# Performance work log

Measured on AMD Instinct MI355X. Metric: run time of the kernel, lower is better.

Reference implementation:

```python
import jax, jax.numpy as jnp
import numpy as np
from jax import lax

B, T = 8, 256
GRID = (8, 8, 8)
X, Y, Z = GRID
N = X * Y * Z            # 512 nodes
C_IN = C_OUT = 8         # 4096 / 512
R = 8                    # num_rand


def _stencil_mask():
    # 7-point stencil mask at kernel center (1,1,1)
    m = np.zeros((3, 3, 3), dtype=np.float32)
    c = 1
    m[c, c, c] = 1.0
    m[c - 1, c, c] = 1.0
    m[c + 1, c, c] = 1.0
    m[c, c - 1, c] = 1.0
    m[c, c + 1, c] = 1.0
    m[c, c, c - 1] = 1.0
    m[c, c, c + 1] = 1.0
    return jnp.asarray(m)


def setup_inputs() -> dict:
    key = jax.random.key(0)
    k1, k2, k3, k4 = jax.random.split(key, 4)
    x = jax.random.normal(k1, (B, T, C_IN * N), dtype=jnp.float32)
    # MaskedConv3d params (kernel 3x3x3)
    fan = C_IN * 27
    conv_w = jax.random.normal(k2, (C_OUT, C_IN, 3, 3, 3), dtype=jnp.float32) / np.sqrt(fan)
    conv_b = jnp.zeros((C_OUT,), dtype=jnp.float32)
    # RandomGraphMixer3D params (xavier-uniform-like)
    bound = np.sqrt(6.0 / (C_IN * R + C_OUT))
    mix_w = jax.random.uniform(k3, (C_OUT, C_IN, R), jnp.float32, -bound, bound)
    mix_b = jnp.zeros((C_OUT,), dtype=jnp.float32)
    rand_indices = jax.random.randint(k4, (N, R), 0, N, dtype=jnp.int32)
    alpha = jnp.float32(0.5)
    return {"x": x, "conv_w": conv_w, "conv_b": conv_b,
            "mix_w": mix_w, "mix_b": mix_b, "alpha": alpha,
            "rand_indices": rand_indices}


def reference(x, conv_w, conv_b, mix_w, mix_b, alpha, rand_indices):
    Bd, Td, D = x.shape
    xt = x.reshape(Bd * Td, C_IN, X, Y, Z)
    # --- masked 7-point stencil conv3d ---
    w = conv_w * _stencil_mask()  # broadcast over (O, I)
    y_local = lax.conv_general_dilated(
        xt, w, window_strides=(1, 1, 1), padding='SAME',
        dimension_numbers=('NCDHW', 'OIDHW', 'NCDHW'))
    y_local = y_local + conv_b[None, :, None, None, None]
    # --- random graph mixer: gather + contract ---
    x_nodes = xt.reshape(Bd * Td, C_IN, N)
    gathered = x_nodes[:, :, rand_indices]              # [BT, C, N, R]
    y_rand = jnp.einsum('ocr,bcnr->bon', mix_w, gathered) + mix_b[None, :, None]
    y_rand = y_rand.reshape(Bd * Td, C_OUT, X, Y, Z)
    # --- sigmoid blend ---
    a = jax.nn.sigmoid(alpha)
    yt = a * y_local + (1.0 - a) * y_rand
    return yt.reshape(Bd, Td, C_OUT * N)
```

## Files before the change

kernel.cpp:

```cpp
#include <hip/hip_runtime.h>
#include <math.h>

#define NNODES 512
#define CIN 8
#define COUT 8
#define RR 8
#define BTB 2
#define GUARD 64
#define SLOTS (GUARD + NNODES + GUARD)
#define SLAB_HW (SLOTS * 8)
#define LDS_HW (BTB * SLAB_HW)
#define WTAB 1024

typedef __attribute__((ext_vector_type(8))) short short8;
typedef __attribute__((ext_vector_type(4))) float floatx4;

__device__ __forceinline__ unsigned int pack_bf16(float a, float b) {
    unsigned int ua = __float_as_uint(a);
    unsigned int ub = __float_as_uint(b);
    ua = (ua + 0x7fffu + ((ua >> 16) & 1u)) >> 16;
    ub = (ub + 0x7fffu + ((ub >> 16) & 1u)) & 0xffff0000u;
    return ua | ub;
}

__global__ void prep(const float* __restrict__ conv_w,
                     const float* __restrict__ conv_b,
                     const float* __restrict__ mix_w,
                     const float* __restrict__ mix_b,
                     const float* __restrict__ alpha_p,
                     const int*   __restrict__ rand_idx,
                     float* __restrict__ ws) {
    const int t = threadIdx.x;
    const float a = 1.0f / (1.0f + expf(-alpha_p[0]));
    if (t < 960) {
        const int oc = t / 15;
        const int tap = t % 15;
        float v;
        if (tap < 7) {
            const int off[7] = {13, 4, 22, 10, 16, 12, 14};
            v = a * conv_w[oc * 27 + off[tap]];
        } else {
            v = (1.0f - a) * mix_w[oc * RR + (tap - 7)];
        }
        ws[t] = v;
    } else if (t < 968) {
        const int o = t - 960;
        ws[960 + o] = a * conv_b[o] + (1.0f - a) * mix_b[o];
    }

    int4* tab = (int4*)((int*)ws + WTAB);
    for (int e = t; e < 2048; e += 1024) {
        const int tt = e >> 6, lane = e & 63;
        const int q = lane >> 4, r16 = lane & 15;
        const int m = tt * 16 + r16;
        const int h = (m >> 3) & 7, w = m & 7;
        int off[4];
#pragma unroll
        for (int i = 0; i < 4; ++i) {
            const int tap = 4 * i + q;
            int o;
            if (tap == 0)       o = GUARD + m;
            else if (tap == 1)  o = GUARD + m - 64;
            else if (tap == 2)  o = GUARD + m + 64;
            else if (tap == 3)  o = (h > 0) ? (GUARD + m - 8) : 0;
            else if (tap == 4)  o = (h < 7) ? (GUARD + m + 8) : 0;
            else if (tap == 5)  o = (w > 0) ? (GUARD + m - 1) : 0;
            else if (tap == 6)  o = (w < 7) ? (GUARD + m + 1) : 0;
            else if (tap <= 14) o = GUARD + rand_idx[m * RR + (tap - 7)];
            else                o = 0;
            off[i] = o * 16;
        }
        tab[e] = make_int4(off[0], off[1], off[2], off[3]);
    }
}

__global__ __launch_bounds__(256) void hybrid3d_v3(
    const float* __restrict__ x,
    const float* __restrict__ wsb,
    float* __restrict__ out)
{
    __shared__ unsigned short lds16[LDS_HW];
    const int tid  = threadIdx.x;
    const int wave = tid >> 6;
    const int lane = tid & 63;
    const int quad = lane >> 4;
    const int r16  = lane & 15;
    const int btl  = wave >> 1;
    const int half = wave & 1;

    {
        const int b = tid >> 7;
        const int s = tid & 127;
        const int slot = (s < GUARD) ? s : (NNODES + s);
        *(uint4*)&lds16[b * SLAB_HW + slot * 8] = make_uint4(0u, 0u, 0u, 0u);
    }

    short8 bfrag[4];
#pragma unroll
    for (int i = 0; i < 4; ++i) {
        const int tap = 4 * i + quad;
        union { unsigned int u[4]; short8 s; } bf;
#pragma unroll
        for (int jp = 0; jp < 4; ++jp) {
            const int c0 = 2 * jp, c1 = 2 * jp + 1;
            float f0 = (r16 < 8 && tap < 15) ? wsb[(r16 * CIN + c0) * 15 + tap] : 0.0f;
            float f1 = (r16 < 8 && tap < 15) ? wsb[(r16 * CIN + c1) * 15 + tap] : 0.0f;
            bf.u[jp] = pack_bf16(f0, f1);
        }
        bfrag[i] = bf.s;
    }
    const float bias = (r16 < 8) ? wsb[960 + r16] : 0.0f;

    const float* xg = x + ((size_t)blockIdx.x * BTB + btl) * (CIN * NNODES);
    unsigned short* slab = lds16 + btl * SLAB_HW;
#pragma unroll
    for (int j = 0; j < 4; ++j) {
        const int n = half * 256 + j * 64 + lane;
        float v[8];
#pragma unroll
        for (int c = 0; c < 8; ++c) v[c] = xg[c * NNODES + n];
        uint4 pk;
        pk.x = pack_bf16(v[0], v[1]);
        pk.y = pack_bf16(v[2], v[3]);
        pk.z = pack_bf16(v[4], v[5]);
        pk.w = pack_bf16(v[6], v[7]);
        *(uint4*)&slab[(GUARD + n) * 8] = pk;
    }
    __syncthreads();

    const char* slabp = (const char*)slab;
    const int4* tab = (const int4*)((const int*)wsb + WTAB);
    float* outb = out + ((size_t)blockIdx.x * BTB + btl) * (COUT * NNODES);

#pragma unroll 2
    for (int tt = 0; tt < 16; ++tt) {
        const int t = half * 16 + tt;
        const int4 off = tab[t * 64 + lane];
        union { uint4 u; short8 s; } r0, r1, r2, r3;
        r0.u = *(const uint4*)(slabp + off.x);
        r1.u = *(const uint4*)(slabp + off.y);
        r2.u = *(const uint4*)(slabp + off.z);
        r3.u = *(const uint4*)(slabp + off.w);

        floatx4 acc_a = {bias, bias, bias, bias};
        floatx4 acc_b = {0.0f, 0.0f, 0.0f, 0.0f};
        acc_a = __builtin_amdgcn_mfma_f32_16x16x32_bf16(r0.s, bfrag[0], acc_a, 0, 0, 0);
        acc_b = __builtin_amdgcn_mfma_f32_16x16x32_bf16(r2.s, bfrag[2], acc_b, 0, 0, 0);
        acc_a = __builtin_amdgcn_mfma_f32_16x16x32_bf16(r1.s, bfrag[1], acc_a, 0, 0, 0);
        acc_b = __builtin_amdgcn_mfma_f32_16x16x32_bf16(r3.s, bfrag[3], acc_b, 0, 0, 0);

        if (r16 < 8) {
            float4 res;
            res.x = acc_a.x + acc_b.x;
            res.y = acc_a.y + acc_b.y;
            res.z = acc_a.z + acc_b.z;
            res.w = acc_a.w + acc_b.w;
            *(float4*)(outb + r16 * NNODES + t * 16 + quad * 4) = res;
        }
    }
}

extern "C" void kernel_launch(void* const* d_in, const int* in_sizes, int n_in,
                              void* d_out, int out_size, void* d_ws, size_t ws_size,
                              hipStream_t stream) {
    const float* x       = (const float*)d_in[0];
    const float* conv_w  = (const float*)d_in[1];
    const float* conv_b  = (const float*)d_in[2];
    const float* mix_w   = (const float*)d_in[3];
    const float* mix_b   = (const float*)d_in[4];
    const float* alpha_p = (const float*)d_in[5];
    const int*   rand_i  = (const int*)d_in[6];
    float* out = (float*)d_out;
    float* ws  = (float*)d_ws;

    const int BT = in_sizes[0] / (CIN * NNODES);

    prep<<<1, 1024, 0, stream>>>(conv_w, conv_b, mix_w, mix_b, alpha_p, rand_i, ws);
    hybrid3d_v3<<<BT / BTB, 256, 0, stream>>>(x, ws, out);
}
```

Baseline: 105.6 us.

## Fold weight prep and offset table into the main kernel, computing offsets inline

Removes the separate single-block prep kernel. The main kernel now computes the sigmoid-blended bf16 weight fragments and bias directly from the raw parameters, and derives the stencil and random-gather LDS offsets in registers instead of reading a precomputed table. The tap-to-lane mapping is reorganized so each quad handles fixed stencil directions, with the random indices prefetched from rand_idx one iteration ahead. This saves a kernel launch and the serialization between the two kernels, at the cost of redundant weight setup in every block and more integer arithmetic per loop iteration.

```diff
diff --git a/kernel.cpp b/kernel.cpp
--- a/kernel.cpp
+++ b/kernel.cpp
@@ -10,7 +10,6 @@
 #define SLOTS (GUARD + NNODES + GUARD)
 #define SLAB_HW (SLOTS * 8)
 #define LDS_HW (BTB * SLAB_HW)
-#define WTAB 1024
 
 typedef __attribute__((ext_vector_type(8))) short short8;
 typedef __attribute__((ext_vector_type(4))) float floatx4;
@@ -23,60 +22,14 @@
     return ua | ub;
 }
 
-__global__ void prep(const float* __restrict__ conv_w,
-                     const float* __restrict__ conv_b,
-                     const float* __restrict__ mix_w,
-                     const float* __restrict__ mix_b,
-                     const float* __restrict__ alpha_p,
-                     const int*   __restrict__ rand_idx,
-                     float* __restrict__ ws) {
-    const int t = threadIdx.x;
-    const float a = 1.0f / (1.0f + expf(-alpha_p[0]));
-    if (t < 960) {
-        const int oc = t / 15;
-        const int tap = t % 15;
-        float v;
-        if (tap < 7) {
-            const int off[7] = {13, 4, 22, 10, 16, 12, 14};
-            v = a * conv_w[oc * 27 + off[tap]];
-        } else {
-            v = (1.0f - a) * mix_w[oc * RR + (tap - 7)];
-        }
-        ws[t] = v;
-    } else if (t < 968) {
-        const int o = t - 960;
-        ws[960 + o] = a * conv_b[o] + (1.0f - a) * mix_b[o];
-    }
-
-    int4* tab = (int4*)((int*)ws + WTAB);
-    for (int e = t; e < 2048; e += 1024) {
-        const int tt = e >> 6, lane = e & 63;
-        const int q = lane >> 4, r16 = lane & 15;
-        const int m = tt * 16 + r16;
-        const int h = (m >> 3) & 7, w = m & 7;
-        int off[4];
-#pragma unroll
-        for (int i = 0; i < 4; ++i) {
-            const int tap = 4 * i + q;
-            int o;
-            if (tap == 0)       o = GUARD + m;
-            else if (tap == 1)  o = GUARD + m - 64;
-            else if (tap == 2)  o = GUARD + m + 64;
-            else if (tap == 3)  o = (h > 0) ? (GUARD + m - 8) : 0;
-            else if (tap == 4)  o = (h < 7) ? (GUARD + m + 8) : 0;
-            else if (tap == 5)  o = (w > 0) ? (GUARD + m - 1) : 0;
-            else if (tap == 6)  o = (w < 7) ? (GUARD + m + 1) : 0;
-            else if (tap <= 14) o = GUARD + rand_idx[m * RR + (tap - 7)];
-            else                o = 0;
-            off[i] = o * 16;
-        }
-        tab[e] = make_int4(off[0], off[1], off[2], off[3]);
-    }
-}
-
-__global__ __launch_bounds__(256) void hybrid3d_v3(
+__global__ __launch_bounds__(256) void hybrid3d_v4(
     const float* __restrict__ x,
-    const float* __restrict__ wsb,
+    const float* __restrict__ conv_w,
+    const float* __restrict__ conv_b,
+    const float* __restrict__ mix_w,
+    const float* __restrict__ mix_b,
+    const float* __restrict__ alpha_p,
+    const int*   __restrict__ rand_idx,
     float* __restrict__ out)
 {
     __shared__ unsigned short lds16[LDS_HW];
@@ -95,22 +48,6 @@
         *(uint4*)&lds16[b * SLAB_HW + slot * 8] = make_uint4(0u, 0u, 0u, 0u);
     }
 
-    short8 bfrag[4];
-#pragma unroll
-    for (int i = 0; i < 4; ++i) {
-        const int tap = 4 * i + quad;
-        union { unsigned int u[4]; short8 s; } bf;
-#pragma unroll
-        for (int jp = 0; jp < 4; ++jp) {
-            const int c0 = 2 * jp, c1 = 2 * jp + 1;
-            float f0 = (r16 < 8 && tap < 15) ? wsb[(r16 * CIN + c0) * 15 + tap] : 0.0f;
-            float f1 = (r16 < 8 && tap < 15) ? wsb[(r16 * CIN + c1) * 15 + tap] : 0.0f;
-            bf.u[jp] = pack_bf16(f0, f1);
-        }
-        bfrag[i] = bf.s;
-    }
-    const float bias = (r16 < 8) ? wsb[960 + r16] : 0.0f;
-
     const float* xg = x + ((size_t)blockIdx.x * BTB + btl) * (CIN * NNODES);
     unsigned short* slab = lds16 + btl * SLAB_HW;
 #pragma unroll
@@ -126,21 +63,80 @@
         pk.w = pack_bf16(v[6], v[7]);
         *(uint4*)&slab[(GUARD + n) * 8] = pk;
     }
+
+    const float aS = 1.0f / (1.0f + expf(-alpha_p[0]));
+    const float aR = 1.0f - aS;
+    short8 bfrag[4];
+#pragma unroll
+    for (int i = 0; i < 4; ++i) {
+        const int tap = 4 * i + quad;
+        union { unsigned int u[4]; short8 s; } bf;
+#pragma unroll
+        for (int jp = 0; jp < 4; ++jp) {
+            float f0 = 0.0f, f1 = 0.0f;
+            if (r16 < 8) {
+                const int c0 = 2 * jp, c1 = c0 + 1;
+                if (tap < 7) {
+                    const unsigned long long TAB =
+                        13ull | (4ull << 8) | (22ull << 16) | (10ull << 24) |
+                        (16ull << 32) | (12ull << 40) | (14ull << 48);
+                    const int co = (int)((TAB >> (8 * tap)) & 0xffull);
+                    f0 = aS * conv_w[(r16 * CIN + c0) * 27 + co];
+                    f1 = aS * conv_w[(r16 * CIN + c1) * 27 + co];
+                } else if (tap < 15) {
+                    const int r = tap - 7;
+                    f0 = aR * mix_w[(r16 * CIN + c0) * RR + r];
+                    f1 = aR * mix_w[(r16 * CIN + c1) * RR + r];
+                }
+            }
+            bf.u[jp] = pack_bf16(f0, f1);
+        }
+        bfrag[i] = bf.s;
+    }
+    const float bias = (r16 < 8) ? (aS * conv_b[r16] + aR * mix_b[r16]) : 0.0f;
+
     __syncthreads();
 
     const char* slabp = (const char*)slab;
-    const int4* tab = (const int4*)((const int*)wsb + WTAB);
     float* outb = out + ((size_t)blockIdx.x * BTB + btl) * (COUT * NNODES);
+
+    const int  w_  = r16 & 7;
+    const int  hb  = r16 >> 3;
+    const int  j1  = (quad + 1) & 3;
+    const bool q3  = (quad == 3);
+    const int  s0d = (quad == 0) ? 0 : (quad == 1) ? -64 : (quad == 2) ? 64 : -8;
+    const int  s1d = (quad == 0) ? 8 : (quad == 1) ? -1 : 1;
+    const bool c1s = (quad == 1) ? (w_ > 0) : (quad == 2) ? (w_ < 7) : true;
+    const int  base0 = (GUARD + r16 + s0d) * 16;
+    const int  base1 = (GUARD + r16 + s1d) * 16;
+
+    const int* rp = rand_idx + ((half * 16) * 16 + r16) * RR + j1;
+    int nr1 = rp[0], nr2 = rp[4];
 
 #pragma unroll 2
     for (int tt = 0; tt < 16; ++tt) {
         const int t = half * 16 + tt;
-        const int4 off = tab[t * 64 + lane];
+        const int rv1 = nr1, rv2 = nr2;
+        if (tt < 15) { rp += 16 * RR; nr1 = rp[0]; nr2 = rp[4]; }
+
+        const int tb = t << 8;
+        const int h  = (2 * t + hb) & 7;
+        int off0 = base0 + tb;
+        if (q3 && h == 0) off0 = 0;
+        const bool ok1 = (quad == 0) ? (h < 7) : c1s;
+        const int off1  = ok1 ? (base1 + tb) : 0;
+        const int offr1 = (GUARD * 16) + (rv1 << 4);
+        const int offr2 = (GUARD * 16) + (rv2 << 4);
+        const int o0 = off0;
+        const int o1 = q3 ? offr1 : off1;
+        const int o2 = q3 ? offr2 : offr1;
+        const int o3 = q3 ? 0 : offr2;
+
         union { uint4 u; short8 s; } r0, r1, r2, r3;
-        r0.u = *(const uint4*)(slabp + off.x);
-        r1.u = *(const uint4*)(slabp + off.y);
-        r2.u = *(const uint4*)(slabp + off.z);
-        r3.u = *(const uint4*)(slabp + off.w);
+        r0.u = *(const uint4*)(slabp + o0);
+        r1.u = *(const uint4*)(slabp + o1);
+        r2.u = *(const uint4*)(slabp + o2);
+        r3.u = *(const uint4*)(slabp + o3);
 
         floatx4 acc_a = {bias, bias, bias, bias};
         floatx4 acc_b = {0.0f, 0.0f, 0.0f, 0.0f};
@@ -171,10 +167,10 @@
     const float* alpha_p = (const float*)d_in[5];
     const int*   rand_i  = (const int*)d_in[6];
     float* out = (float*)d_out;
-    float* ws  = (float*)d_ws;
+    (void)d_ws; (void)ws_size;
 
     const int BT = in_sizes[0] / (CIN * NNODES);
 
-    prep<<<1, 1024, 0, stream>>>(conv_w, conv_b, mix_w, mix_b, alpha_p, rand_i, ws);
-    hybrid3d_v3<<<BT / BTB, 256, 0, stream>>>(x, ws, out);
+    hybrid3d_v4<<<BT / BTB, 256, 0, stream>>>(x, conv_w, conv_b, mix_w, mix_b,
+                                              alpha_p, rand_i, out);
 }
```

After: 112.6 us. 1.07x slower.
